# Performance work log

Measured on AMD Instinct MI355X. Metric: run time of the kernel, lower is better.

## Reference

```python
import jax, jax.numpy as jnp
import numpy as np

CURVS = (-1.0, 0.0, 1.0, -0.5)
N, E, B = 50000, 800000, 128
IN, HID, OUT, GHID = 128, 128, 128, 32
K = len(CURVS)
TAU_MIN, TAU_MAX = 0.05, 10.0
EPS = 1e-15


def _vnorm(x):
    return jnp.maximum(jnp.linalg.norm(x, axis=-1, keepdims=True), EPS)


def tan_k(x, k):
    if k > 0:
        sk = np.sqrt(k)
        return jnp.tan(x * sk) / sk
    if k < 0:
        sk = np.sqrt(-k)
        return jnp.tanh(x * sk) / sk
    return x


def artan_k(x, k):
    if k > 0:
        sk = np.sqrt(k)
        return jnp.arctan(x * sk) / sk
    if k < 0:
        sk = np.sqrt(-k)
        return jnp.arctanh(jnp.clip(x * sk, -1.0 + 1e-7, 1.0 - 1e-7)) / sk
    return x


def project(x, k):
    # clip inside Poincare ball for k<0; identity otherwise (geoopt Stereographic.projx)
    if k < 0:
        maxn = (1.0 - 1e-5) / np.sqrt(-k)
        n = _vnorm(x)
        return jnp.where(n > maxn, x * (maxn / n), x)
    return x


def expmap0(u, k):
    n = _vnorm(u)
    return project(tan_k(n, k) * u / n, k)


def logmap0(y, k):
    n = _vnorm(y)
    return artan_k(n, k) * y / n


def mobius_add(x, y, k):
    x2 = jnp.sum(x * x, -1, keepdims=True)
    y2 = jnp.sum(y * y, -1, keepdims=True)
    xy = jnp.sum(x * y, -1, keepdims=True)
    num = (1.0 - 2.0 * k * xy - k * y2) * x + (1.0 + k * x2) * y
    den = jnp.maximum(1.0 - 2.0 * k * xy + k * k * x2 * y2, 1e-15)
    return project(num / den, k)


def mobius_matvec(W, x, k):
    mx = x @ W.T
    if k == 0:
        return mx
    xn = _vnorm(x)
    mxn = _vnorm(mx)
    res = tan_k(mxn / xn * artan_k(xn, k), k) * mx / mxn
    res = jnp.where(jnp.sum(jnp.abs(mx), -1, keepdims=True) == 0.0, 0.0, res)
    return project(res, k)


def dist(x, y, k):
    return 2.0 * artan_k(_vnorm(mobius_add(-x, y, k)), k)[..., 0]


def setup_inputs():
    key = jax.random.key(0)
    ks = jax.random.split(key, 12)
    x = jax.random.normal(ks[0], (N, IN), jnp.float32)
    edge_index = jax.random.randint(ks[1], (2, E), 0, N)
    batch = jnp.sort(jax.random.randint(ks[2], (N,), 0, B))
    s1 = float(np.sqrt(2.0 / (IN + HID)))
    s2 = float(np.sqrt(2.0 / (HID + OUT)))
    sg1 = float(np.sqrt(2.0 / (IN + GHID)))
    sg2 = float(np.sqrt(2.0 / (GHID + OUT)))
    raw0 = float(np.log(np.expm1(1.0 - TAU_MIN)))
    return {
        "x": x,
        "edge_index": edge_index,
        "batch": batch,
        "expert_w1": jax.random.normal(ks[3], (K, HID, IN), jnp.float32) * s1,
        "expert_b1": jnp.zeros((K, HID), jnp.float32),
        "expert_w2": jax.random.normal(ks[4], (K, OUT, HID), jnp.float32) * s2,
        "expert_b2": jnp.zeros((K, OUT), jnp.float32),
        "gate_w1": jax.random.normal(ks[5], (GHID, IN), jnp.float32) * sg1,
        "gate_b1": jnp.zeros((GHID,), jnp.float32),
        "gate_w2": jax.random.normal(ks[6], (OUT, GHID), jnp.float32) * sg2,
        "gate_b2": jnp.zeros((OUT,), jnp.float32),
        "gate_u": jax.random.normal(ks[7], (K, OUT), jnp.float32) * 0.02,
        "tau_raw": jnp.full((K,), raw0, jnp.float32),
    }


def _graph_norm(edge_index):
    loops = jnp.arange(N)
    row = jnp.concatenate([edge_index[0], loops])
    col = jnp.concatenate([edge_index[1], loops])
    deg = jax.ops.segment_sum(jnp.ones(E + N, jnp.float32), col, num_segments=N)
    dinv = deg ** -0.5  # deg >= 1 due to self loops
    return row, col, dinv[row] * dinv[col]


def _kappa_conv(xm, W, b, row, col, enorm, k):
    h = mobius_matvec(W, xm, k)
    bias_pt = expmap0(b[None, :], k)  # proju at origin is identity
    h = mobius_add(h, bias_pt, k)
    t = logmap0(h, k)  # [N, out]
    agg = jax.ops.segment_sum(enorm[:, None] * t[row], col, num_segments=N)
    return expmap0(agg, k)


def reference(x, edge_index, batch, expert_w1, expert_b1, expert_w2, expert_b2,
              gate_w1, gate_b1, gate_w2, gate_b2, gate_u, tau_raw):
    x = x.astype(jnp.float32)
    row, col, enorm = _graph_norm(edge_index)
    counts = jnp.maximum(
        jax.ops.segment_sum(jnp.ones(N, jnp.float32), batch, num_segments=B), 1.0)[:, None]

    # --- Riemannian experts ---
    embs = []
    for i, kv in enumerate(CURVS):
        xm = expmap0(x, kv)  # manifold init (proju at origin = identity)
        xm = _kappa_conv(xm, expert_w1[i], expert_b1[i], row, col, enorm, kv)
        xm = _kappa_conv(xm, expert_w2[i], expert_b2[i], row, col, enorm, kv)
        z = logmap0(xm, kv)
        embs.append(jax.ops.segment_sum(z, batch, num_segments=B) / counts)
    features = jnp.concatenate(embs, axis=-1)  # [B, K*OUT]

    # --- Euclidean gating encoder (GCN) ---
    def gcn(h, W, b):
        m = (h @ W.T)
        out = jax.ops.segment_sum(enorm[:, None] * m[row], col, num_segments=N) + b
        return jax.nn.relu(out)

    g = gcn(x, gate_w1, gate_b1)
    g = gcn(g, gate_w2, gate_b2)
    hgate = jax.ops.segment_sum(g, batch, num_segments=B) / counts  # [B, OUT]

    # --- Geometric distance gate ---
    tau = jnp.clip(jax.nn.softplus(tau_raw) + TAU_MIN, TAU_MIN, TAU_MAX)
    dists = []
    for i, kv in enumerate(CURVS):
        zk = expmap0(hgate, kv)
        yk = expmap0(gate_u[i][None, :], kv)
        dists.append(dist(zk, yk, kv))
    dists = jnp.stack(dists, axis=-1)  # [B, K]
    weights = jax.nn.softmax(-dists / tau[None, :], axis=-1)

    scaled = features * jnp.repeat(weights, OUT, axis=1)
    return scaled, weights, dists, tau
```

## Files before the change

### kernel.cpp

```cpp
#include <hip/hip_runtime.h>
#include <math.h>

#define NN 50000
#define EE 800000
#define ETOT (EE + NN)
#define BB 128
#define DIM 128
#define GHID 32
#define CHUNK 128
#define NCHUNK ((ETOT + CHUNK - 1) / CHUNK)
#define SCB 196

#define DEGB 3125
#define G1B 782
#define W2HB 512
#define MEGA0B (DEGB + G1B + W2HB + 1 + 8)
#define PLACEB 3321
#define BNB ((NCHUNK + 255) / 256)

typedef _Float16 f16;
typedef _Float16 f16x2 __attribute__((ext_vector_type(2)));
typedef _Float16 f16x8 __attribute__((ext_vector_type(8)));
typedef float f32x4 __attribute__((ext_vector_type(4)));

struct CurvPack {
  float k[4], sk[4], mx[4], thr2[4];
};

__device__ __forceinline__ float wsum64(float v) {
#pragma unroll
  for (int m = 32; m; m >>= 1) v += __shfl_xor(v, m, 64);
  return v;
}

__device__ __forceinline__ float tan_k_d(float x, float kv, float sk) {
  if (kv > 0.f) return tanf(x * sk) / sk;
  if (kv < 0.f) return tanhf(x * sk) / sk;
  return x;
}

__device__ __forceinline__ float artan_k_d(float x, float kv, float sk) {
  if (kv > 0.f) return atanf(x * sk) / sk;
  if (kv < 0.f) {
    float t = x * sk;
    t = fminf(fmaxf(t, -1.f + 1e-7f), 1.f - 1e-7f);
    return atanhf(t) / sk;
  }
  return x;
}

__device__ __forceinline__ float proj_scale_d(float n, float kv, float maxn) {
  if (kv < 0.f && n > maxn) return maxn / n;
  return 1.f;
}

__global__ __launch_bounds__(256) void k_mega0(
    const int* __restrict__ ei, float* __restrict__ deg, const int* __restrict__ batch,
    int* __restrict__ boff, float* __restrict__ counts, const float* __restrict__ eb1,
    const float* __restrict__ eb2, float* __restrict__ biasb, const float* __restrict__ ew1,
    const float* __restrict__ ew2, f16* __restrict__ whi, f16* __restrict__ wlo,
    const float* __restrict__ x, const float* __restrict__ gw1, float* __restrict__ m1,
    CurvPack cp) {
  __shared__ float smem[64 * 68 + 64 * 36];
  int bx = blockIdx.x;
  int tid = threadIdx.x;

  if (bx < DEGB) {
    int i = bx * 256 + tid;
    if (i < EE) atomicAdd(&deg[ei[EE + i]], 1.0f);
    return;
  }
  bx -= DEGB;

  if (bx < G1B) {
    float(*xT)[68] = (float(*)[68])smem;
    float(*Wt)[36] = (float(*)[36])(smem + 64 * 68);
    int n0 = bx * 64;
    int c = tid & 7, r = tid >> 3;
    float acc[2][4];
#pragma unroll
    for (int i = 0; i < 2; i++)
#pragma unroll
      for (int jj = 0; jj < 4; jj++) acc[i][jj] = 0.f;
    for (int kc = 0; kc < 2; kc++) {
      if (kc) __syncthreads();
#pragma unroll
      for (int it = 0; it < 8; it++) {
        int u = tid + it * 256;
        int j = u >> 6, kd = u & 63;
        Wt[kd][j] = gw1[j * 128 + kc * 64 + kd];
      }
#pragma unroll
      for (int it = 0; it < 4; it++) {
        int u = tid + it * 256;
        int node = u >> 4, c4 = u & 15;
        float4 v = make_float4(0.f, 0.f, 0.f, 0.f);
        if (n0 + node < NN) v = ((const float4*)x)[(size_t)(n0 + node) * 32 + kc * 16 + c4];
        xT[4 * c4 + 0][node] = v.x;
        xT[4 * c4 + 1][node] = v.y;
        xT[4 * c4 + 2][node] = v.z;
        xT[4 * c4 + 3][node] = v.w;
      }
      __syncthreads();
#pragma unroll 8
      for (int kd = 0; kd < 64; kd++) {
        float2 av = *(const float2*)&xT[kd][r * 2];
        float4 bv = *(const float4*)&Wt[kd][c * 4];
        float a[2] = {av.x, av.y};
        float bbv[4] = {bv.x, bv.y, bv.z, bv.w};
#pragma unroll
        for (int i = 0; i < 2; i++)
#pragma unroll
          for (int jj = 0; jj < 4; jj++) acc[i][jj] = fmaf(a[i], bbv[jj], acc[i][jj]);
      }
    }
#pragma unroll
    for (int i = 0; i < 2; i++) {
      int node = n0 + r * 2 + i;
      if (node >= NN) continue;
      ((float4*)m1)[(size_t)node * 8 + c] =
          make_float4(acc[i][0], acc[i][1], acc[i][2], acc[i][3]);
    }
    return;
  }
  bx -= G1B;

  if (bx < W2HB) {
    int i = bx * 256 + tid;
    if (i >= 8 * 16384) return;
    int slot = i >> 14;
    int r = i & 16383;
    int ex = slot >> 1, layer = slot & 1;
    float w = (layer ? ew2 : ew1)[ex * 16384 + r];
    f16 h = (f16)w;
    whi[i] = h;
    wlo[i] = (f16)(w - (float)h);
    return;
  }
  bx -= W2HB;

  if (bx == 0) {
    int b = tid;
    if (b <= 128) {
      int lo = 0, hi = NN;
      while (lo < hi) {
        int mid = (lo + hi) >> 1;
        if (batch[mid] < b) lo = mid + 1; else hi = mid;
      }
      boff[b] = lo;
    }
    __syncthreads();
    if (b < 128) counts[b] = (float)(boff[b + 1] - boff[b]);
    return;
  }
  bx -= 1;

  {
    float* l2 = smem;
    int ex = bx >> 1, layer = bx & 1;
    float kv = cp.k[ex], sk = cp.sk[ex], maxn = cp.mx[ex];
    const float* b = (layer ? eb2 : eb1) + ex * 128;
    float* outb = biasb + bx * 132;
    int j = tid;
    float v = (j < 128) ? b[j] : 0.f;
    float n2 = wsum64(v * v);
    if ((j & 63) == 0) l2[j >> 6] = n2;
    __syncthreads();
    n2 = l2[0] + l2[1];
    float nraw = sqrtf(n2);
    float nnv = fmaxf(nraw, 1e-15f);
    float tk = tan_k_d(nnv, kv, sk);
    float s = tk / nnv;
    float pn = fmaxf(fabsf(tk) * (nraw / nnv), 1e-15f);
    float ps = proj_scale_d(pn, kv, maxn);
    float bp = ps * s * v;
    if (j < 128) outb[j] = bp;
    float y2v = wsum64(bp * bp);
    __syncthreads();
    if ((j & 63) == 0) l2[j >> 6] = y2v;
    __syncthreads();
    if (j == 0) outb[128] = l2[0] + l2[1];
  }
}

__global__ void k_dinv(float* __restrict__ deg, int* __restrict__ ideg, int n) {
  int i = blockIdx.x * 256 + threadIdx.x;
  if (i < n) {
    float d = deg[i] + 1.0f;
    ideg[i] = (int)(d + 0.5f);
    deg[i] = 1.0f / sqrtf(d);
  }
}

__global__ void k_scanA(const int* __restrict__ ideg, int* __restrict__ bsum, int n) {
  __shared__ int ls[4];
  int i = blockIdx.x * 256 + threadIdx.x;
  int v = (i < n) ? ideg[i] : 0;
#pragma unroll
  for (int m = 1; m < 64; m <<= 1) v += __shfl_xor(v, m, 64);
  if ((threadIdx.x & 63) == 0) ls[threadIdx.x >> 6] = v;
  __syncthreads();
  if (threadIdx.x == 0) bsum[blockIdx.x] = ls[0] + ls[1] + ls[2] + ls[3];
}

__global__ void k_scanB(int* __restrict__ bsum, int nb) {
  __shared__ int wsh[4];
  int tid = threadIdx.x;
  int lane = tid & 63, w = tid >> 6;
  int v = (tid < nb) ? bsum[tid] : 0;
  int x = v;
#pragma unroll
  for (int o = 1; o < 64; o <<= 1) {
    int t = __shfl_up(x, o, 64);
    if (lane >= o) x += t;
  }
  if (lane == 63) wsh[w] = x;
  __syncthreads();
  int add = 0;
  for (int k2 = 0; k2 < w; k2++) add += wsh[k2];
  if (tid < nb) bsum[tid] = add + x - v;
}

__global__ void k_scanC(const int* __restrict__ ideg, const int* __restrict__ bsum,
                        int* __restrict__ off, int* __restrict__ cursor, int n) {
  __shared__ int wsh[4];
  int i = blockIdx.x * 256 + threadIdx.x;
  int lane = threadIdx.x & 63, w = threadIdx.x >> 6;
  int v = (i < n) ? ideg[i] : 0;
  int x = v;
#pragma unroll
  for (int o = 1; o < 64; o <<= 1) {
    int t = __shfl_up(x, o, 64);
    if (lane >= o) x += t;
  }
  if (lane == 63) wsh[w] = x;
  __syncthreads();
  int add = bsum[blockIdx.x];
  for (int k2 = 0; k2 < w; k2++) add += wsh[k2];
  int excl = add + x - v;
  if (i < n) {
    off[i] = excl;
    cursor[i] = excl;
  }
  if (i == n - 1) off[n] = excl + v;
}

__global__ void k_megapre(const int* __restrict__ ei, const float* __restrict__ dinv,
                          int* __restrict__ cursor, int2* __restrict__ esw,
                          const int* __restrict__ off, int* __restrict__ bnode,
                          int* __restrict__ bslot) {
  int bx = blockIdx.x;
  if (bx < PLACEB) {
    int i = bx * 256 + threadIdx.x;
    if (i >= ETOT) return;
    int r_, c_;
    if (i < EE) {
      r_ = ei[i];
      c_ = ei[EE + i];
    } else {
      r_ = i - EE;
      c_ = i - EE;
    }
    int p = atomicAdd(&cursor[c_], 1);
    esw[p] = make_int2(r_, __float_as_int(dinv[r_] * dinv[c_]));
    return;
  }
  bx -= PLACEB;
  int g = bx * 256 + threadIdx.x;
  if (g >= NCHUNK) return;
  int e0 = g * CHUNK;
  int lo = 0, hi = NN;
  while (hi - lo > 1) {
    int mid = (lo + hi) >> 1;
    if (off[mid] <= e0) lo = mid; else hi = mid;
  }
  bnode[g] = lo;
  bslot[g] = (off[lo] + CHUNK - 1) / CHUNK;
}

__device__ __forceinline__ bool span_head(const int* bnode, const int* bslot, const int* off,
                                          int g, int& nd) {
  if (bslot[g] != g) return false;
  nd = bnode[g];
  int s = off[nd], e = off[nd + 1];
  return (s / CHUNK) != ((e - 1) / CHUNK);
}

__global__ __launch_bounds__(256) void k_matmfma(
    const float* __restrict__ A, int astr, int aoffPerEx,
    const f16* __restrict__ whiB, const f16* __restrict__ wloB,
    const float* __restrict__ biasB, int layer, f16* __restrict__ tout, int n,
    const int* __restrict__ bnode, const int* __restrict__ bslot,
    const int* __restrict__ off, float* __restrict__ aggc, CurvPack cp) {
  if (blockIdx.y == 4) {
    int g = blockIdx.x * 4 + (threadIdx.x >> 6);
    int lane = threadIdx.x & 63;
    if (g >= NCHUNK) return;
    int nd;
    if (!span_head(bnode, bslot, off, g, nd)) return;
    float2 z = make_float2(0.f, 0.f);
#pragma unroll
    for (int i = 0; i < 5; i++) ((float2*)aggc)[(size_t)g * 320 + i * 64 + lane] = z;
    return;
  }
  __shared__ float red[3][16][4];
  __shared__ float redT[16][4];
  __shared__ float nAs[16], nCs[16], nL[16];
  int ex = blockIdx.y;
  float kv = cp.k[ex], sk = cp.sk[ex], maxn = cp.mx[ex];
  const f16* whi = whiB + (size_t)(ex * 2 + layer) * 16384;
  const f16* wlo = wloB + (size_t)(ex * 2 + layer) * 16384;
  const float* biasb = biasB + (ex * 2 + layer) * 132;

  int tid = threadIdx.x;
  int w = tid >> 6;
  int lane = tid & 63;
  int col = lane & 15;
  int quad = lane >> 4;
  int n0w = blockIdx.x * 16;
  if (n0w >= n) return;

  int anodec = min(n0w + col, n - 1);
  const float* arow = A + (size_t)anodec * astr + ex * aoffPerEx;
  int jt0 = w * 2;

  f32x4 acc[2];
  acc[0] = (f32x4){0.f, 0.f, 0.f, 0.f};
  acc[1] = (f32x4){0.f, 0.f, 0.f, 0.f};
  float a_n2 = 0.f;

#pragma unroll
  for (int kc = 0; kc < 4; kc++) {
    int kb = kc * 32 + quad * 8;
    float4 a0 = *(const float4*)(arow + kb);
    float4 a1 = *(const float4*)(arow + kb + 4);
    float av[8] = {a0.x, a0.y, a0.z, a0.w, a1.x, a1.y, a1.z, a1.w};
    f16x8 Ah, Al;
#pragma unroll
    for (int i = 0; i < 8; i++) {
      a_n2 = fmaf(av[i], av[i], a_n2);
      f16 h = (f16)av[i];
      Ah[i] = h;
      Al[i] = (f16)(av[i] - (float)h);
    }
#pragma unroll
    for (int j2 = 0; j2 < 2; j2++) {
      const f16* bh = whi + (size_t)((jt0 + j2) * 16 + col) * 128 + kb;
      const f16* bl = wlo + (size_t)((jt0 + j2) * 16 + col) * 128 + kb;
      f16x8 Bh = *(const f16x8*)bh;
      f16x8 Bl = *(const f16x8*)bl;
      acc[j2] = __builtin_amdgcn_mfma_f32_16x16x32_f16(Ah, Bh, acc[j2], 0, 0, 0);
      acc[j2] = __builtin_amdgcn_mfma_f32_16x16x32_f16(Ah, Bl, acc[j2], 0, 0, 0);
      acc[j2] = __builtin_amdgcn_mfma_f32_16x16x32_f16(Al, Bh, acc[j2], 0, 0, 0);
    }
  }
  a_n2 += __shfl_xor(a_n2, 16, 64);
  a_n2 += __shfl_xor(a_n2, 32, 64);

  float bpj[2];
  bpj[0] = biasb[jt0 * 16 + col];
  bpj[1] = biasb[(jt0 + 1) * 16 + col];
  float y2 = biasb[128];

#pragma unroll
  for (int r = 0; r < 4; r++) {
    float s0 = 0.f, s1 = 0.f, s2 = 0.f;
#pragma unroll
    for (int j2 = 0; j2 < 2; j2++) {
      float v = acc[j2][r];
      s0 = fmaf(v, v, s0);
      s1 += fabsf(v);
      s2 = fmaf(v, bpj[j2], s2);
    }
#pragma unroll
    for (int m = 1; m < 16; m <<= 1) {
      s0 += __shfl_xor(s0, m, 64);
      s1 += __shfl_xor(s1, m, 64);
      s2 += __shfl_xor(s2, m, 64);
    }
    if (col == 0) {
      red[0][quad * 4 + r][w] = s0;
      red[1][quad * 4 + r][w] = s1;
      red[2][quad * 4 + r][w] = s2;
    }
  }
  __syncthreads();

  if (tid < 16) {
    float nraw0 = sqrtf(a_n2);
    float nnv0 = fmaxf(nraw0, 1e-15f);
    float tk0 = tan_k_d(nnv0, kv, sk);
    float pn0 = fmaxf(fabsf(tk0) * (nraw0 / nnv0), 1e-15f);
    float ps0 = proj_scale_d(pn0, kv, maxn);
    float sc = (tk0 / nnv0) * ps0;
    float xnr = pn0 * ps0;

    float s0f = (red[0][tid][0] + red[0][tid][1] + red[0][tid][2] + red[0][tid][3]) * sc * sc;
    float s1f = (red[1][tid][0] + red[1][tid][1] + red[1][tid][2] + red[1][tid][3]) * fabsf(sc);
    float s2f = (red[2][tid][0] + red[2][tid][1] + red[2][tid][2] + red[2][tid][3]) * sc;
    float xn = fmaxf(xnr, 1e-15f);
    float mxraw = sqrtf(s0f);
    float mxv = fmaxf(mxraw, 1e-15f);
    float ar = artan_k_d(xn, kv, sk);
    float c1 = tan_k_d(mxv / xn * ar, kv, sk);
    float s = (s1f == 0.f) ? 0.f : c1 / mxv;
    float pn = fmaxf(fabsf(c1) * (mxraw / mxv), 1e-15f);
    float ps = (s1f == 0.f) ? 1.f : proj_scale_d(pn, kv, maxn);
    s *= ps;
    float x2 = (s * s) * s0f;
    float xy = s * s2f;
    float Aa = 1.f - 2.f * kv * xy - kv * y2;
    float Cc = 1.f + kv * x2;
    float den = fmaxf(1.f - 2.f * kv * xy + (kv * kv) * x2 * y2, 1e-15f);
    nAs[tid] = Aa * s / den * sc;
    nCs[tid] = Cc / den;
  }
  __syncthreads();

#pragma unroll
  for (int r = 0; r < 4; r++) {
    int idx = quad * 4 + r;
    float Asc = nAs[idx], Cs = nCs[idx];
    float t0 = 0.f;
#pragma unroll
    for (int j2 = 0; j2 < 2; j2++) {
      float v = fmaf(Asc, acc[j2][r], Cs * bpj[j2]);
      t0 = fmaf(v, v, t0);
    }
#pragma unroll
    for (int m = 1; m < 16; m <<= 1) t0 += __shfl_xor(t0, m, 64);
    if (col == 0) redT[idx][w] = t0;
  }
  __syncthreads();

  if (tid < 16) {
    float t0f = redT[tid][0] + redT[tid][1] + redT[tid][2] + redT[tid][3];
    float nraw = sqrtf(t0f);
    float ps2 = proj_scale_d(fmaxf(nraw, 1e-15f), kv, maxn);
    float nh = fmaxf(ps2 * nraw, 1e-15f);
    nL[tid] = artan_k_d(nh, kv, sk) / nh * ps2;
  }
  __syncthreads();

#pragma unroll
  for (int r = 0; r < 4; r++) {
    int idx = quad * 4 + r;
    int gnode = n0w + idx;
    if (gnode >= n) continue;
    float Asc = nAs[idx], Cs = nCs[idx], L = nL[idx];
    f16* trow = tout + (size_t)gnode * 512;
#pragma unroll
    for (int j2 = 0; j2 < 2; j2++) {
      float v = fmaf(Asc, acc[j2][r], Cs * bpj[j2]);
      int d = (jt0 + j2) * 16 + col;
      trow[(d >> 1) * 8 + ex * 2 + (d & 1)] = (f16)(L * v);
    }
  }
}

template <int MODE>
__global__ __launch_bounds__(256) void k_aggF(
    const int2* __restrict__ esw, const int* __restrict__ off,
    const int* __restrict__ bnode, const int* __restrict__ bslot,
    const int* __restrict__ batch, const f16x8* __restrict__ t,
    const float* __restrict__ gsrc, float* __restrict__ agg1, float* __restrict__ aggc,
    float* __restrict__ g1out, float* __restrict__ feats,
    const float* __restrict__ gbias, const float* __restrict__ gw2,
    float* __restrict__ hgate, int etot, CurvPack cp) {
  __shared__ float gw2s[(MODE == 1) ? 32 : 1][128];
  if (MODE == 1) {
#pragma unroll
    for (int i2 = 0; i2 < 16; i2++) {
      int u = threadIdx.x + i2 * 256;
      gw2s[u >> 7][u & 127] = gw2[(u & 127) * 32 + (u >> 7)];
    }
    __syncthreads();
  }
  int gw = blockIdx.x * 4 + (threadIdx.x >> 6);
  int lane = threadIdx.x & 63;
  int e0 = gw * CHUNK;
  if (e0 >= etot) return;
  int e1 = min(e0 + CHUNK, etot);
  int lane31 = lane & 31;
  int bnHead = bnode[gw];
  int slotA = bslot[gw];
  int slotB = ((gw + 1) * CHUNK < etot) ? bslot[gw + 1] : slotA;

  int2 mv0 = esw[min(e0 + lane, etot - 1)];
  int2 mv1 = esw[min(e0 + 64 + lane, etot - 1)];
  int offv = off[min(bnHead + lane, NN)];
  int batchv = 0;
  if (MODE == 1) batchv = batch[min(bnHead + lane, NN - 1)];

  int cur = bnHead;
  int runStart = __builtin_amdgcn_readlane(offv, 0);
  int eend = __builtin_amdgcn_readlane(offv, 1);

  auto nextOff = [&](int c1) -> int {
    int rel = c1 - bnHead;
    if (rel < 64) return __builtin_amdgcn_readlane(offv, rel);
    return off[c1];
  };
  auto curBatch = [&](int c) -> int {
    int rel = c - bnHead;
    if (rel < 64) return __builtin_amdgcn_readlane(batchv, rel);
    return batch[c];
  };

  float ax[4], ay[4], pax[4], pay[4];
#pragma unroll
  for (int e = 0; e < 4; e++) ax[e] = ay[e] = pax[e] = pay[e] = 0.f;
  float gx = 0.f, pgx = 0.f, pgy = 0.f;
  int bcur = (MODE == 1) ? __builtin_amdgcn_readlane(batchv, 0) : 0;
  float bbx, bby = 0.f;
  if (MODE == 0) {
    bbx = gbias[lane31];
  } else {
    float2 bb = ((const float2*)gbias)[lane];
    bbx = bb.x;
    bby = bb.y;
  }

  auto flushInterior = [&]() {
#pragma unroll
    for (int e = 0; e < 4; e++) {
      if (MODE == 0) {
        ((float2*)agg1)[(size_t)cur * 256 + e * 64 + lane] = make_float2(ax[e], ay[e]);
      } else {
        float n2 = wsum64(fmaf(ax[e], ax[e], ay[e] * ay[e]));
        if (n2 <= cp.thr2[e]) {
          pax[e] += ax[e];
          pay[e] += ay[e];
        } else {
          float nraw = sqrtf(n2);
          float nnv = fmaxf(nraw, 1e-15f);
          float tk = tan_k_d(nnv, cp.k[e], cp.sk[e]);
          float s = tk / nnv;
          float pn = fmaxf(fabsf(tk) * (nraw / nnv), 1e-15f);
          float ps = proj_scale_d(pn, cp.k[e], cp.mx[e]);
          s *= ps;
          float nh = fmaxf(pn * ps, 1e-15f);
          float sc = artan_k_d(nh, cp.k[e], cp.sk[e]) / nh * s;
          pax[e] = fmaf(sc, ax[e], pax[e]);
          pay[e] = fmaf(sc, ay[e], pay[e]);
        }
      }
    }
    if (MODE == 0) {
      if (lane < 32) g1out[(size_t)cur * 32 + lane] = fmaxf(gx + bbx, 0.f);
    } else {
      float o0 = 0.f, o1 = 0.f;
#pragma unroll
      for (int k2 = 0; k2 < 32; k2++) {
        float agk = __int_as_float(__builtin_amdgcn_readlane(__float_as_int(gx), k2));
        float2 wv = *(const float2*)&gw2s[k2][lane * 2];
        o0 = fmaf(agk, wv.x, o0);
        o1 = fmaf(agk, wv.y, o1);
      }
      pgx += fmaxf(o0 + bbx, 0.f);
      pgy += fmaxf(o1 + bby, 0.f);
    }
  };
  auto flushBoundary = [&]() {
    int slot = (cur == bnHead) ? slotA : slotB;
    float* dp = aggc + (size_t)slot * 640;
#pragma unroll
    for (int e = 0; e < 4; e++) {
      atomicAdd(dp + e * 128 + lane * 2, ax[e]);
      atomicAdd(dp + e * 128 + lane * 2 + 1, ay[e]);
    }
    if (lane < 32) atomicAdd(dp + 512 + lane, gx);
  };
  auto flushPool = [&]() {
#pragma unroll
    for (int e = 0; e < 4; e++) {
      float* fp = &feats[(size_t)bcur * 512 + e * 128 + lane * 2];
      atomicAdd(fp, pax[e]);
      atomicAdd(fp + 1, pay[e]);
    }
    float* hp = &hgate[(size_t)bcur * 128 + lane * 2];
    atomicAdd(hp, pgx);
    atomicAdd(hp + 1, pgy);
  };

  f16x8 rv[8];
  float gf[8];

#pragma unroll
  for (int b = 0; b < CHUNK / 8; b++) {
    int jb = e0 + b * 8;
    if (jb < e1) {
      const int2 mvsel = (b < 8) ? mv0 : mv1;
#pragma unroll
      for (int q = 0; q < 8; q++) {
        int s = __builtin_amdgcn_readlane(mvsel.x, (b & 7) * 8 + q);
        rv[q] = t[(size_t)s * 64 + lane];
        gf[q] = gsrc[(size_t)s * 32 + lane31];
      }
#pragma unroll
      for (int q = 0; q < 8; q++) {
        if (jb + q == eend) {
          if (runStart >= e0) flushInterior(); else flushBoundary();
#pragma unroll
          for (int e = 0; e < 4; e++) ax[e] = ay[e] = 0.f;
          gx = 0.f;
          runStart = jb + q;
          cur++;
          eend = nextOff(cur + 1);
          if (MODE == 1) {
            int nbt = curBatch(cur);
            if (nbt != bcur) {
              flushPool();
#pragma unroll
              for (int e = 0; e < 4; e++) pax[e] = pay[e] = 0.f;
              pgx = pgy = 0.f;
              bcur = nbt;
            }
          }
        }
        float w = __int_as_float(__builtin_amdgcn_readlane(mvsel.y, (b & 7) * 8 + q));
#pragma unroll
        for (int e = 0; e < 4; e++) {
          ax[e] = fmaf(w, (float)rv[q][2 * e], ax[e]);
          ay[e] = fmaf(w, (float)rv[q][2 * e + 1], ay[e]);
        }
        gx = fmaf(w, gf[q], gx);
      }
    }
  }
  if (runStart >= e0 && eend <= e1) flushInterior(); else flushBoundary();
  if (MODE == 1) flushPool();
}

__global__ void k_fix1(const int* __restrict__ bnode, const int* __restrict__ bslot,
                       const int* __restrict__ off, const float* __restrict__ aggc,
                       float* __restrict__ agg1, float* __restrict__ g1,
                       const float* __restrict__ gb1, int nchunk) {
  int g = blockIdx.x * 4 + (threadIdx.x >> 6);
  int lane = threadIdx.x & 63;
  if (g >= nchunk) return;
  int nd;
  if (!span_head(bnode, bslot, off, g, nd)) return;
  const float* sp = aggc + (size_t)g * 640;
#pragma unroll
  for (int e = 0; e < 4; e++) {
    float2 v = ((const float2*)sp)[e * 64 + lane];
    ((float2*)agg1)[(size_t)nd * 256 + e * 64 + lane] = v;
  }
  if (lane < 32) g1[(size_t)nd * 32 + lane] = fmaxf(sp[512 + lane] + gb1[lane], 0.f);
}

__global__ void k_fix2(const int* __restrict__ bnode, const int* __restrict__ bslot,
                       const int* __restrict__ off, const float* __restrict__ aggc,
                       const int* __restrict__ batch, float* __restrict__ feats,
                       const float* __restrict__ gb2, const float* __restrict__ gw2,
                       float* __restrict__ hgate, int nchunk, CurvPack cp) {
  int g = blockIdx.x * 4 + (threadIdx.x >> 6);
  int lane = threadIdx.x & 63;
  if (g >= nchunk) return;
  int nd;
  if (!span_head(bnode, bslot, off, g, nd)) return;
  int b = batch[nd];
  const float* sp = aggc + (size_t)g * 640;
#pragma unroll
  for (int e = 0; e < 4; e++) {
    float2 v = ((const float2*)sp)[e * 64 + lane];
    float n2 = wsum64(fmaf(v.x, v.x, v.y * v.y));
    float nraw = sqrtf(n2);
    float nnv = fmaxf(nraw, 1e-15f);
    float tk = tan_k_d(nnv, cp.k[e], cp.sk[e]);
    float s = tk / nnv;
    float pn = fmaxf(fabsf(tk) * (nraw / nnv), 1e-15f);
    float ps = proj_scale_d(pn, cp.k[e], cp.mx[e]);
    s *= ps;
    float nh = fmaxf(pn * ps, 1e-15f);
    float sc = artan_k_d(nh, cp.k[e], cp.sk[e]) / nh * s;
    float* fp = &feats[(size_t)b * 512 + e * 128 + lane * 2];
    atomicAdd(fp, sc * v.x);
    atomicAdd(fp + 1, sc * v.y);
  }
  float2 bb = ((const float2*)gb2)[lane];
  float o0 = 0.f, o1 = 0.f;
#pragma unroll 8
  for (int k2 = 0; k2 < 32; k2++) {
    float agk = sp[512 + k2];
    o0 = fmaf(agk, gw2[(2 * lane) * 32 + k2], o0);
    o1 = fmaf(agk, gw2[(2 * lane + 1) * 32 + k2], o1);
  }
  float* hp = &hgate[(size_t)b * 128 + lane * 2];
  atomicAdd(hp, fmaxf(o0 + bb.x, 0.f));
  atomicAdd(hp + 1, fmaxf(o1 + bb.y, 0.f));
}

__global__ __launch_bounds__(128) void k_final(const float* __restrict__ feats,
                                               const float* __restrict__ hgate,
                                               const float* __restrict__ counts,
                                               const float* __restrict__ gate_u,
                                               const float* __restrict__ tau_raw,
                                               float* __restrict__ out, CurvPack cp) {
  __shared__ float l2[2];
  int b = blockIdx.x;
  int j = threadIdx.x;
  float cnt = fmaxf(counts[b], 1.f);
  float hg = hgate[(size_t)b * 128 + j] / cnt;

  auto bsum = [&](float v) -> float {
    v = wsum64(v);
    __syncthreads();
    if ((j & 63) == 0) l2[j >> 6] = v;
    __syncthreads();
    return l2[0] + l2[1];
  };

  float nhg2 = bsum(hg * hg);
  float nhgraw = sqrtf(nhg2);
  float nhg = fmaxf(nhgraw, 1e-15f);

  float d[4], tau[4];
#pragma unroll
  for (int i = 0; i < 4; i++) {
    float kv = cp.k[i], sk = cp.sk[i], mxn = cp.mx[i];
    float tk = tan_k_d(nhg, kv, sk);
    float s = tk / nhg;
    float pn = fmaxf(fabsf(tk) * (nhgraw / nhg), 1e-15f);
    s *= proj_scale_d(pn, kv, mxn);
    float zk = s * hg;

    float u = gate_u[i * 128 + j];
    float nu2 = bsum(u * u);
    float nuraw = sqrtf(nu2);
    float nu = fmaxf(nuraw, 1e-15f);
    float tku = tan_k_d(nu, kv, sk);
    float su = tku / nu;
    float pnu = fmaxf(fabsf(tku) * (nuraw / nu), 1e-15f);
    su *= proj_scale_d(pnu, kv, mxn);
    float yk = su * u;

    float xv = -zk;
    float x2 = bsum(xv * xv);
    float y2 = bsum(yk * yk);
    float xy = bsum(xv * yk);
    float A = 1.f - 2.f * kv * xy - kv * y2;
    float C = 1.f + kv * x2;
    float den = fmaxf(1.f - 2.f * kv * xy + (kv * kv) * x2 * y2, 1e-15f);
    float ma = (A * xv + C * yk) / den;
    float m2 = bsum(ma * ma);
    float mraw = sqrtf(m2);
    float ps2 = proj_scale_d(fmaxf(mraw, 1e-15f), kv, mxn);
    float nm = fmaxf(ps2 * mraw, 1e-15f);
    d[i] = 2.f * artan_k_d(nm, kv, sk);

    float tr = tau_raw[i];
    tau[i] = fminf(fmaxf(log1pf(expf(tr)) + 0.05f, 0.05f), 10.f);
  }

  float xi[4];
  float mxv = -1e30f;
#pragma unroll
  for (int i = 0; i < 4; i++) {
    xi[i] = -d[i] / tau[i];
    mxv = fmaxf(mxv, xi[i]);
  }
  float es = 0.f, e[4];
#pragma unroll
  for (int i = 0; i < 4; i++) {
    e[i] = expf(xi[i] - mxv);
    es += e[i];
  }
  float w[4];
#pragma unroll
  for (int i = 0; i < 4; i++) w[i] = e[i] / es;

#pragma unroll
  for (int i = 0; i < 4; i++)
    out[(size_t)b * 512 + i * 128 + j] = feats[(size_t)b * 512 + i * 128 + j] / cnt * w[i];

  if (j < 4) {
    out[65536 + b * 4 + j] = w[j];
    out[66048 + b * 4 + j] = d[j];
  }
  if (b == 0 && j < 4) out[66560 + j] = tau[j];
}

extern "C" void kernel_launch(void* const* d_in, const int* in_sizes, int n_in,
                              void* d_out, int out_size, void* d_ws, size_t ws_size,
                              hipStream_t stream) {
  const float* x = (const float*)d_in[0];
  const int* ei = (const int*)d_in[1];
  const int* batch = (const int*)d_in[2];
  const float* ew1 = (const float*)d_in[3];
  const float* eb1 = (const float*)d_in[4];
  const float* ew2 = (const float*)d_in[5];
  const float* eb2 = (const float*)d_in[6];
  const float* gw1 = (const float*)d_in[7];
  const float* gb1 = (const float*)d_in[8];
  const float* gw2 = (const float*)d_in[9];
  const float* gb2 = (const float*)d_in[10];
  const float* gu = (const float*)d_in[11];
  const float* traw = (const float*)d_in[12];
  float* out = (float*)d_out;

  const int N = NN, E = EE, ET = ETOT, B = BB;

  float* ws = (float*)d_ws;
  size_t o = 0;
  f16* t4 = (f16*)ws;       o += (size_t)N * 256;
  float* agg1 = ws + o;     o += (size_t)N * 512;
  float* aggc = ws + o;     o += (size_t)NCHUNK * 640;
  float* deg = ws + o;      o += N;
  float* counts = ws + o;   o += 256;
  float* feats = ws + o;    o += (size_t)B * 512;
  float* hg = ws + o;       o += (size_t)B * 128;
  float* biasb = ws + o;    o += 8 * 132;
  f16* whi = (f16*)(ws + o);    o += 8 * 16384 / 2;
  f16* wlo = (f16*)(ws + o);    o += 8 * 16384 / 2;
  float* m1 = ws + o;       o += (size_t)N * 32;
  float* g1 = ws + o;       o += (size_t)N * 32;
  int* ideg = (int*)(ws + o);   o += N;
  int* csroff = (int*)(ws + o); o += N + 8;
  int* cursor = (int*)(ws + o); o += N;
  int* boff = (int*)(ws + o);   o += 136;
  int* bsum = (int*)(ws + o);   o += 256;
  int* bnode = (int*)(ws + o);  o += NCHUNK + 8;
  int* bslot = (int*)(ws + o);  o += NCHUNK + 8;
  int2* esw = (int2*)(ws + o);  o += (size_t)2 * ET;

  hipMemsetAsync(deg, 0, ((size_t)N + 256 + (size_t)B * 512 + (size_t)B * 128) * sizeof(float),
                 stream);

  const double curvs[4] = {-1.0, 0.0, 1.0, -0.5};
  CurvPack cp;
  for (int i = 0; i < 4; i++) {
    double kd = curvs[i];
    double skd = sqrt(fabs(kd));
    cp.k[i] = (float)kd;
    cp.sk[i] = (float)skd;
    cp.mx[i] = (kd < 0) ? (float)((1.0 - 1e-5) / skd) : 3.0e38f;
    if (kd < 0) {
      double thr = 6.0 / skd;
      cp.thr2[i] = (float)(thr * thr);
    } else if (kd > 0) {
      double thr = 1.5 / skd;
      cp.thr2[i] = (float)(thr * thr);
    } else {
      cp.thr2[i] = 3.0e38f;
    }
  }

  k_mega0<<<MEGA0B, 256, 0, stream>>>(ei, deg, batch, boff, counts, eb1, eb2, biasb, ew1, ew2,
                                      whi, wlo, x, gw1, m1, cp);
  k_dinv<<<SCB, 256, 0, stream>>>(deg, ideg, N);
  k_scanA<<<SCB, 256, 0, stream>>>(ideg, bsum, N);
  k_scanB<<<1, 256, 0, stream>>>(bsum, SCB);
  k_scanC<<<SCB, 256, 0, stream>>>(ideg, bsum, csroff, cursor, N);
  k_megapre<<<PLACEB + BNB, 256, 0, stream>>>(ei, deg, cursor, esw, csroff, bnode, bslot);

  const int aggBlocks = (NCHUNK + 3) / 4;
  dim3 mfmaGrid((N + 15) / 16, 5);

  k_matmfma<<<mfmaGrid, 256, 0, stream>>>(x, 128, 0, whi, wlo, biasb, 0, t4, N, bnode, bslot,
                                          csroff, aggc, cp);
  k_aggF<0><<<aggBlocks, 256, 0, stream>>>(esw, csroff, bnode, bslot, batch, (const f16x8*)t4,
                                           m1, agg1, aggc, g1, nullptr, gb1, nullptr, nullptr,
                                           ET, cp);
  k_fix1<<<aggBlocks, 256, 0, stream>>>(bnode, bslot, csroff, aggc, agg1, g1, gb1, NCHUNK);

  k_matmfma<<<mfmaGrid, 256, 0, stream>>>(agg1, 512, 128, whi, wlo, biasb, 1, t4, N, bnode,
                                          bslot, csroff, aggc, cp);
  k_aggF<1><<<aggBlocks, 256, 0, stream>>>(esw, csroff, bnode, bslot, batch, (const f16x8*)t4,
                                           g1, nullptr, aggc, nullptr, feats, gb2, gw2, hg, ET,
                                           cp);
  k_fix2<<<aggBlocks, 256, 0, stream>>>(bnode, bslot, csroff, aggc, batch, feats, gb2, gw2, hg,
                                        NCHUNK, cp);

  k_final<<<B, 128, 0, stream>>>(feats, hg, counts, gu, traw, out, cp);

  (void)in_sizes; (void)n_in; (void)out_size; (void)ws_size;
}
```

Baseline: 911.6 us.

## Split edge aggregation into two expert-pair passes with half-width feature layout

The transformed feature table is stored as two separate planes, one per pair of experts, instead of one interleaved 512-wide row per node. Each aggregation kernel now runs twice, once per plane, so every gathered row is 256 halves and the random-access working set per pass is halved. The intent is to fit the gathered table better in cache during the irregular edge gather. In exchange, the edge lists, offsets and batch data are read twice, and there are two extra kernel launches.

```diff
diff --git a/kernel.cpp b/kernel.cpp
--- a/kernel.cpp
+++ b/kernel.cpp
@@ -20,6 +20,7 @@
 
 typedef _Float16 f16;
 typedef _Float16 f16x2 __attribute__((ext_vector_type(2)));
+typedef _Float16 f16x4 __attribute__((ext_vector_type(4)));
 typedef _Float16 f16x8 __attribute__((ext_vector_type(8)));
 typedef float f32x4 __attribute__((ext_vector_type(4)));
 
@@ -442,33 +443,35 @@
   }
   __syncthreads();
 
+  f16* tp = tout + (size_t)(ex >> 1) * NN * 256;
+  int slot = ex & 1;
 #pragma unroll
   for (int r = 0; r < 4; r++) {
     int idx = quad * 4 + r;
     int gnode = n0w + idx;
     if (gnode >= n) continue;
     float Asc = nAs[idx], Cs = nCs[idx], L = nL[idx];
-    f16* trow = tout + (size_t)gnode * 512;
+    f16* trow = tp + (size_t)gnode * 256;
 #pragma unroll
     for (int j2 = 0; j2 < 2; j2++) {
       float v = fmaf(Asc, acc[j2][r], Cs * bpj[j2]);
       int d = (jt0 + j2) * 16 + col;
-      trow[(d >> 1) * 8 + ex * 2 + (d & 1)] = (f16)(L * v);
-    }
-  }
-}
-
-template <int MODE>
+      trow[(d >> 1) * 4 + slot * 2 + (d & 1)] = (f16)(L * v);
+    }
+  }
+}
+
+template <int MODE, int PASS>
 __global__ __launch_bounds__(256) void k_aggF(
     const int2* __restrict__ esw, const int* __restrict__ off,
     const int* __restrict__ bnode, const int* __restrict__ bslot,
-    const int* __restrict__ batch, const f16x8* __restrict__ t,
+    const int* __restrict__ batch, const f16* __restrict__ tbase,
     const float* __restrict__ gsrc, float* __restrict__ agg1, float* __restrict__ aggc,
     float* __restrict__ g1out, float* __restrict__ feats,
     const float* __restrict__ gbias, const float* __restrict__ gw2,
     float* __restrict__ hgate, int etot, CurvPack cp) {
-  __shared__ float gw2s[(MODE == 1) ? 32 : 1][128];
-  if (MODE == 1) {
+  __shared__ float gw2s[(MODE == 1 && PASS == 0) ? 32 : 1][128];
+  if (MODE == 1 && PASS == 0) {
 #pragma unroll
     for (int i2 = 0; i2 < 16; i2++) {
       int u = threadIdx.x + i2 * 256;
@@ -476,6 +479,7 @@
     }
     __syncthreads();
   }
+  const f16x4* t = (const f16x4*)(tbase + (size_t)PASS * NN * 256);
   int gw = blockIdx.x * 4 + (threadIdx.x >> 6);
   int lane = threadIdx.x & 63;
   int e0 = gw * CHUNK;
@@ -507,83 +511,94 @@
     return batch[c];
   };
 
-  float ax[4], ay[4], pax[4], pay[4];
-#pragma unroll
-  for (int e = 0; e < 4; e++) ax[e] = ay[e] = pax[e] = pay[e] = 0.f;
+  float ax[2], ay[2], pax[2], pay[2];
+#pragma unroll
+  for (int e = 0; e < 2; e++) ax[e] = ay[e] = pax[e] = pay[e] = 0.f;
   float gx = 0.f, pgx = 0.f, pgy = 0.f;
   int bcur = (MODE == 1) ? __builtin_amdgcn_readlane(batchv, 0) : 0;
-  float bbx, bby = 0.f;
-  if (MODE == 0) {
-    bbx = gbias[lane31];
-  } else {
-    float2 bb = ((const float2*)gbias)[lane];
-    bbx = bb.x;
-    bby = bb.y;
+  float bbx = 0.f, bby = 0.f;
+  if (PASS == 0) {
+    if (MODE == 0) {
+      bbx = gbias[lane31];
+    } else {
+      float2 bb = ((const float2*)gbias)[lane];
+      bbx = bb.x;
+      bby = bb.y;
+    }
   }
 
   auto flushInterior = [&]() {
 #pragma unroll
-    for (int e = 0; e < 4; e++) {
+    for (int e = 0; e < 2; e++) {
+      const int ge = PASS * 2 + e;
       if (MODE == 0) {
-        ((float2*)agg1)[(size_t)cur * 256 + e * 64 + lane] = make_float2(ax[e], ay[e]);
+        ((float2*)agg1)[(size_t)cur * 256 + ge * 64 + lane] = make_float2(ax[e], ay[e]);
       } else {
         float n2 = wsum64(fmaf(ax[e], ax[e], ay[e] * ay[e]));
-        if (n2 <= cp.thr2[e]) {
+        if (n2 <= cp.thr2[ge]) {
           pax[e] += ax[e];
           pay[e] += ay[e];
         } else {
           float nraw = sqrtf(n2);
           float nnv = fmaxf(nraw, 1e-15f);
-          float tk = tan_k_d(nnv, cp.k[e], cp.sk[e]);
+          float tk = tan_k_d(nnv, cp.k[ge], cp.sk[ge]);
           float s = tk / nnv;
           float pn = fmaxf(fabsf(tk) * (nraw / nnv), 1e-15f);
-          float ps = proj_scale_d(pn, cp.k[e], cp.mx[e]);
+          float ps = proj_scale_d(pn, cp.k[ge], cp.mx[ge]);
           s *= ps;
           float nh = fmaxf(pn * ps, 1e-15f);
-          float sc = artan_k_d(nh, cp.k[e], cp.sk[e]) / nh * s;
+          float sc = artan_k_d(nh, cp.k[ge], cp.sk[ge]) / nh * s;
           pax[e] = fmaf(sc, ax[e], pax[e]);
           pay[e] = fmaf(sc, ay[e], pay[e]);
         }
       }
     }
-    if (MODE == 0) {
-      if (lane < 32) g1out[(size_t)cur * 32 + lane] = fmaxf(gx + bbx, 0.f);
-    } else {
-      float o0 = 0.f, o1 = 0.f;
-#pragma unroll
-      for (int k2 = 0; k2 < 32; k2++) {
-        float agk = __int_as_float(__builtin_amdgcn_readlane(__float_as_int(gx), k2));
-        float2 wv = *(const float2*)&gw2s[k2][lane * 2];
-        o0 = fmaf(agk, wv.x, o0);
-        o1 = fmaf(agk, wv.y, o1);
+    if (PASS == 0) {
+      if (MODE == 0) {
+        if (lane < 32) g1out[(size_t)cur * 32 + lane] = fmaxf(gx + bbx, 0.f);
+      } else {
+        float o0 = 0.f, o1 = 0.f;
+#pragma unroll
+        for (int k2 = 0; k2 < 32; k2++) {
+          float agk = __int_as_float(__builtin_amdgcn_readlane(__float_as_int(gx), k2));
+          float2 wv = *(const float2*)&gw2s[k2][lane * 2];
+          o0 = fmaf(agk, wv.x, o0);
+          o1 = fmaf(agk, wv.y, o1);
+        }
+        pgx += fmaxf(o0 + bbx, 0.f);
+        pgy += fmaxf(o1 + bby, 0.f);
       }
-      pgx += fmaxf(o0 + bbx, 0.f);
-      pgy += fmaxf(o1 + bby, 0.f);
     }
   };
   auto flushBoundary = [&]() {
     int slot = (cur == bnHead) ? slotA : slotB;
     float* dp = aggc + (size_t)slot * 640;
 #pragma unroll
-    for (int e = 0; e < 4; e++) {
-      atomicAdd(dp + e * 128 + lane * 2, ax[e]);
-      atomicAdd(dp + e * 128 + lane * 2 + 1, ay[e]);
-    }
-    if (lane < 32) atomicAdd(dp + 512 + lane, gx);
+    for (int e = 0; e < 2; e++) {
+      const int ge = PASS * 2 + e;
+      atomicAdd(dp + ge * 128 + lane * 2, ax[e]);
+      atomicAdd(dp + ge * 128 + lane * 2 + 1, ay[e]);
+    }
+    if (PASS == 0) {
+      if (lane < 32) atomicAdd(dp + 512 + lane, gx);
+    }
   };
   auto flushPool = [&]() {
 #pragma unroll
-    for (int e = 0; e < 4; e++) {
-      float* fp = &feats[(size_t)bcur * 512 + e * 128 + lane * 2];
+    for (int e = 0; e < 2; e++) {
+      const int ge = PASS * 2 + e;
+      float* fp = &feats[(size_t)bcur * 512 + ge * 128 + lane * 2];
       atomicAdd(fp, pax[e]);
       atomicAdd(fp + 1, pay[e]);
     }
-    float* hp = &hgate[(size_t)bcur * 128 + lane * 2];
-    atomicAdd(hp, pgx);
-    atomicAdd(hp + 1, pgy);
+    if (PASS == 0) {
+      float* hp = &hgate[(size_t)bcur * 128 + lane * 2];
+      atomicAdd(hp, pgx);
+      atomicAdd(hp + 1, pgy);
+    }
   };
 
-  f16x8 rv[8];
+  f16x4 rv[8];
   float gf[8];
 
 #pragma unroll
@@ -595,14 +610,14 @@
       for (int q = 0; q < 8; q++) {
         int s = __builtin_amdgcn_readlane(mvsel.x, (b & 7) * 8 + q);
         rv[q] = t[(size_t)s * 64 + lane];
-        gf[q] = gsrc[(size_t)s * 32 + lane31];
+        if (PASS == 0) gf[q] = gsrc[(size_t)s * 32 + lane31];
       }
 #pragma unroll
       for (int q = 0; q < 8; q++) {
         if (jb + q == eend) {
           if (runStart >= e0) flushInterior(); else flushBoundary();
 #pragma unroll
-          for (int e = 0; e < 4; e++) ax[e] = ay[e] = 0.f;
+          for (int e = 0; e < 2; e++) ax[e] = ay[e] = 0.f;
           gx = 0.f;
           runStart = jb + q;
           cur++;
@@ -612,7 +627,7 @@
             if (nbt != bcur) {
               flushPool();
 #pragma unroll
-              for (int e = 0; e < 4; e++) pax[e] = pay[e] = 0.f;
+              for (int e = 0; e < 2; e++) pax[e] = pay[e] = 0.f;
               pgx = pgy = 0.f;
               bcur = nbt;
             }
@@ -620,11 +635,11 @@
         }
         float w = __int_as_float(__builtin_amdgcn_readlane(mvsel.y, (b & 7) * 8 + q));
 #pragma unroll
-        for (int e = 0; e < 4; e++) {
+        for (int e = 0; e < 2; e++) {
           ax[e] = fmaf(w, (float)rv[q][2 * e], ax[e]);
           ay[e] = fmaf(w, (float)rv[q][2 * e + 1], ay[e]);
         }
-        gx = fmaf(w, gf[q], gx);
+        if (PASS == 0) gx = fmaf(w, gf[q], gx);
       }
     }
   }
@@ -860,16 +875,20 @@
 
   k_matmfma<<<mfmaGrid, 256, 0, stream>>>(x, 128, 0, whi, wlo, biasb, 0, t4, N, bnode, bslot,
                                           csroff, aggc, cp);
-  k_aggF<0><<<aggBlocks, 256, 0, stream>>>(esw, csroff, bnode, bslot, batch, (const f16x8*)t4,
-                                           m1, agg1, aggc, g1, nullptr, gb1, nullptr, nullptr,
-                                           ET, cp);
+  k_aggF<0, 0><<<aggBlocks, 256, 0, stream>>>(esw, csroff, bnode, bslot, batch, t4, m1, agg1,
+                                              aggc, g1, nullptr, gb1, nullptr, nullptr, ET, cp);
+  k_aggF<0, 1><<<aggBlocks, 256, 0, stream>>>(esw, csroff, bnode, bslot, batch, t4, nullptr,
+                                              agg1, aggc, nullptr, nullptr, nullptr, nullptr,
+                                              nullptr, ET, cp);
   k_fix1<<<aggBlocks, 256, 0, stream>>>(bnode, bslot, csroff, aggc, agg1, g1, gb1, NCHUNK);
 
   k_matmfma<<<mfmaGrid, 256, 0, stream>>>(agg1, 512, 128, whi, wlo, biasb, 1, t4, N, bnode,
                                           bslot, csroff, aggc, cp);
-  k_aggF<1><<<aggBlocks, 256, 0, stream>>>(esw, csroff, bnode, bslot, batch, (const f16x8*)t4,
-                                           g1, nullptr, aggc, nullptr, feats, gb2, gw2, hg, ET,
-                                           cp);
+  k_aggF<1, 0><<<aggBlocks, 256, 0, stream>>>(esw, csroff, bnode, bslot, batch, t4, g1, nullptr,
+                                              aggc, nullptr, feats, gb2, gw2, hg, ET, cp);
+  k_aggF<1, 1><<<aggBlocks, 256, 0, stream>>>(esw, csroff, bnode, bslot, batch, t4, nullptr,
+                                              nullptr, aggc, nullptr, feats, nullptr, nullptr,
+                                              nullptr, ET, cp);
   k_fix2<<<aggBlocks, 256, 0, stream>>>(bnode, bslot, csroff, aggc, batch, feats, gb2, gw2, hg,
                                         NCHUNK, cp);
 
```

Result: no change. 912.6 us (+0.1%).
